# Optimization experiments

Hardware: AMD Instinct MI355X
Metric: run time of the kernel (lower is better)

## Reference

```python
import jax, jax.numpy as jnp
import numpy as np

N_NODES = 100000
N_EDGES = 600000
D_IN = 128   # num_features (== hidden due to source-code quirk)
D_H = 128    # hidden
BN_EPS = 1e-5
NORM_EPS = 1e-12


def _sage_conv(x, Wl, bl, Wr, src, dst):
    # mean aggregation of neighbor messages x_j (j = src) at target i (dst)
    msg_sum = jax.ops.segment_sum(x[src], dst, num_segments=N_NODES)          # [N, D]
    deg = jax.ops.segment_sum(jnp.ones_like(dst, dtype=x.dtype), dst,
                              num_segments=N_NODES)                            # [N]
    mean = msg_sum / jnp.maximum(deg, 1.0)[:, None]
    out = mean @ Wl.T + bl + x @ Wr.T   # lin_l(aggr) + lin_r(x)
    # F.normalize(out, p=2, dim=-1)
    norm = jnp.linalg.norm(out, axis=-1, keepdims=True)
    return out / jnp.maximum(norm, NORM_EPS)


def setup_inputs() -> dict:
    key = jax.random.key(0)
    ks = jax.random.split(key, 10)
    s1 = 1.0 / np.sqrt(D_IN)
    s2 = 1.0 / np.sqrt(D_H)
    x = jax.random.normal(ks[0], (N_NODES, D_IN), dtype=jnp.float32)
    edge_index = jax.random.randint(ks[1], (2, N_EDGES), 0, N_NODES, dtype=jnp.int64)
    return {
        "x": x,
        "edge_index": edge_index,
        "Wl1": jax.random.uniform(ks[2], (D_H, D_IN), jnp.float32, -s1, s1),
        "bl1": jax.random.uniform(ks[3], (D_H,), jnp.float32, -s1, s1),
        "Wr1": jax.random.uniform(ks[4], (D_H, D_IN), jnp.float32, -s1, s1),
        "Wl2": jax.random.uniform(ks[5], (D_H, D_H), jnp.float32, -s2, s2),
        "bl2": jax.random.uniform(ks[6], (D_H,), jnp.float32, -s2, s2),
        "Wr2": jax.random.uniform(ks[7], (D_H, D_H), jnp.float32, -s2, s2),
        "bn_gamma": jnp.ones((D_H,), jnp.float32),
        "bn_beta": jnp.zeros((D_H,), jnp.float32),
        "bn_mean": jax.random.normal(ks[8], (D_H,), jnp.float32) * 0.1,
        "bn_var": jnp.abs(jax.random.normal(ks[9], (D_H,), jnp.float32)) + 0.5,
    }


def reference(x, edge_index, Wl1, bl1, Wr1, Wl2, bl2, Wr2,
              bn_gamma, bn_beta, bn_mean, bn_var):
    src, dst = edge_index[0], edge_index[1]
    x1 = _sage_conv(x, Wl1, bl1, Wr1, src, dst)  # computed, unused (as in source)
    # transition applied to original x (source-code quirk): ReLU -> BN(eval) -> Dropout(id)
    h = jax.nn.relu(x)
    h = (h - bn_mean) * jax.lax.rsqrt(bn_var + BN_EPS) * bn_gamma + bn_beta
    x2 = _sage_conv(h, Wl2, bl2, Wr2, src, dst)
    return x2
```

## Files before the change

kernel.cpp:

```cpp
#include <hip/hip_runtime.h>
#include <math.h>

#define NN 100000
#define NE 600000
#define DD 128
#define NTILES 6250
#define TPB 8

typedef __attribute__((ext_vector_type(8))) __bf16 bf16x8;
typedef __attribute__((ext_vector_type(4))) float f32x4;

__device__ inline unsigned short f2bf(float f) {
    unsigned int u = __float_as_uint(f);
    unsigned int r = (u + 0x7fffu + ((u >> 16) & 1u)) >> 16;
    return (unsigned short)r;
}

__global__ void hist_kernel(const int* __restrict__ ei, int* __restrict__ counts) {
    int e = blockIdx.x * blockDim.x + threadIdx.x;
    if (e < NE) atomicAdd(&counts[ei[NE + e]], 1);
}

__global__ __launch_bounds__(256) void scan1_kernel(const int* __restrict__ counts,
                                                    int* __restrict__ offsets,
                                                    int* __restrict__ partials, int n) {
    __shared__ int tmp[256];
    int i = blockIdx.x * 256 + threadIdx.x;
    int v = (i < n) ? counts[i] : 0;
    tmp[threadIdx.x] = v;
    __syncthreads();
    for (int off = 1; off < 256; off <<= 1) {
        int t = (threadIdx.x >= off) ? tmp[threadIdx.x - off] : 0;
        __syncthreads();
        tmp[threadIdx.x] += t;
        __syncthreads();
    }
    if (i < n) offsets[i] = tmp[threadIdx.x] - v;
    if (threadIdx.x == 255) partials[blockIdx.x] = tmp[255];
}

__global__ __launch_bounds__(512) void scan2_kernel(int* __restrict__ partials, int nb) {
    __shared__ int tmp[512];
    int v = (threadIdx.x < nb) ? partials[threadIdx.x] : 0;
    tmp[threadIdx.x] = v;
    __syncthreads();
    for (int off = 1; off < 512; off <<= 1) {
        int t = (threadIdx.x >= off) ? tmp[threadIdx.x - off] : 0;
        __syncthreads();
        tmp[threadIdx.x] += t;
        __syncthreads();
    }
    if (threadIdx.x < nb) partials[threadIdx.x] = tmp[threadIdx.x] - v;
}

__global__ void scan3_kernel(int* __restrict__ offsets, int* __restrict__ cursor,
                             const int* __restrict__ partials, int n) {
    int i = blockIdx.x * 256 + threadIdx.x;
    if (i < n) {
        int o = offsets[i] + partials[blockIdx.x];
        offsets[i] = o;
        cursor[i]  = o;
    }
    if (i == 0) offsets[n] = NE;
}

__global__ void reorder_kernel(const int* __restrict__ ei, int* __restrict__ cursor,
                               int* __restrict__ ssrc) {
    int e = blockIdx.x * blockDim.x + threadIdx.x;
    if (e < NE) {
        int pos = atomicAdd(&cursor[ei[NE + e]], 1);
        ssrc[pos] = ei[e];
    }
}

__global__ void wt_stage_kernel(const float* __restrict__ Wl2,
                                const float* __restrict__ Wr2,
                                unsigned short* __restrict__ WT) {
    int t = blockIdx.x * blockDim.x + threadIdx.x;
    if (t >= DD * 256) return;
    int n = t >> 8;
    int k = t & 255;
    float v = (k < DD) ? Wl2[n * DD + k] : Wr2[n * DD + (k - DD)];
    WT[t] = f2bf(v);
}

__global__ __launch_bounds__(256) void aggregate_kernel(
    const float* __restrict__ x, const int* __restrict__ offsets,
    const int* __restrict__ ssrc,
    const float* __restrict__ bn_gamma, const float* __restrict__ bn_beta,
    const float* __restrict__ bn_mean, const float* __restrict__ bn_var,
    unsigned short* __restrict__ A)
{
    const int node = blockIdx.x * 8 + (threadIdx.x >> 5);
    const int l = threadIdx.x & 31;
    const int c = l * 4;

    const float4 bm = *(const float4*)(bn_mean  + c);
    const float4 bv = *(const float4*)(bn_var   + c);
    const float4 bg = *(const float4*)(bn_gamma + c);
    const float4 bb = *(const float4*)(bn_beta  + c);
    const float sc0 = rsqrtf(bv.x + 1e-5f) * bg.x;
    const float sc1 = rsqrtf(bv.y + 1e-5f) * bg.y;
    const float sc2 = rsqrtf(bv.z + 1e-5f) * bg.z;
    const float sc3 = rsqrtf(bv.w + 1e-5f) * bg.w;

    const int st = offsets[node], en = offsets[node + 1];
    const float* xb = x + c;

    float s0 = 0.f, s1 = 0.f, s2 = 0.f, s3 = 0.f;
    int j = st;
    for (; j + 4 <= en; j += 4) {
        const int4 ss = *(const int4*)(ssrc + j);
        float4 v0 = *(const float4*)(xb + (size_t)ss.x * DD);
        float4 v1 = *(const float4*)(xb + (size_t)ss.y * DD);
        float4 v2 = *(const float4*)(xb + (size_t)ss.z * DD);
        float4 v3 = *(const float4*)(xb + (size_t)ss.w * DD);
        s0 += fmaxf(v0.x, 0.f) + fmaxf(v1.x, 0.f) + fmaxf(v2.x, 0.f) + fmaxf(v3.x, 0.f);
        s1 += fmaxf(v0.y, 0.f) + fmaxf(v1.y, 0.f) + fmaxf(v2.y, 0.f) + fmaxf(v3.y, 0.f);
        s2 += fmaxf(v0.z, 0.f) + fmaxf(v1.z, 0.f) + fmaxf(v2.z, 0.f) + fmaxf(v3.z, 0.f);
        s3 += fmaxf(v0.w, 0.f) + fmaxf(v1.w, 0.f) + fmaxf(v2.w, 0.f) + fmaxf(v3.w, 0.f);
    }
    for (; j < en; ++j) {
        int s = ssrc[j];
        float4 v = *(const float4*)(xb + (size_t)s * DD);
        s0 += fmaxf(v.x, 0.f);
        s1 += fmaxf(v.y, 0.f);
        s2 += fmaxf(v.z, 0.f);
        s3 += fmaxf(v.w, 0.f);
    }

    const int deg = en - st;
    float m0, m1, m2, m3;
    if (deg > 0) {
        float inv = 1.0f / (float)deg;
        m0 = (s0 * inv - bm.x) * sc0 + bb.x;
        m1 = (s1 * inv - bm.y) * sc1 + bb.y;
        m2 = (s2 * inv - bm.z) * sc2 + bb.z;
        m3 = (s3 * inv - bm.w) * sc3 + bb.w;
    } else {
        m0 = m1 = m2 = m3 = 0.f;
    }

    const float4 xv = *(const float4*)(xb + (size_t)node * DD);
    float h0 = (fmaxf(xv.x, 0.f) - bm.x) * sc0 + bb.x;
    float h1 = (fmaxf(xv.y, 0.f) - bm.y) * sc1 + bb.y;
    float h2 = (fmaxf(xv.z, 0.f) - bm.z) * sc2 + bb.z;
    float h3 = (fmaxf(xv.w, 0.f) - bm.w) * sc3 + bb.w;

    unsigned short* arow = A + (size_t)node * 256;
    ushort4 mm; mm.x = f2bf(m0); mm.y = f2bf(m1); mm.z = f2bf(m2); mm.w = f2bf(m3);
    ushort4 hh; hh.x = f2bf(h0); hh.y = f2bf(h1); hh.z = f2bf(h2); hh.w = f2bf(h3);
    *(ushort4*)(arow + c)      = mm;
    *(ushort4*)(arow + DD + c) = hh;
}

__global__ __launch_bounds__(256) void mfma_gemm_norm_kernel(
    const unsigned short* __restrict__ A, const unsigned short* __restrict__ WT,
    const float* __restrict__ bl, float* __restrict__ out)
{
    __shared__ float partial[4][16];

    const int wave = threadIdx.x >> 6;
    const int l    = threadIdx.x & 63;
    const int r    = l & 15;
    const int seg  = l >> 4;
    const int c0   = wave * 32;

    bf16x8 bf0[8], bf1[8];
    {
        const unsigned short* bp0 = WT + (size_t)(c0 + r) * 256 + seg * 8;
        const unsigned short* bp1 = WT + (size_t)(c0 + 16 + r) * 256 + seg * 8;
#pragma unroll
        for (int kk = 0; kk < 8; ++kk) {
            bf0[kk] = *(const bf16x8*)(bp0 + kk * 32);
            bf1[kk] = *(const bf16x8*)(bp1 + kk * 32);
        }
    }
    const float bias0 = bl[c0 + r];
    const float bias1 = bl[c0 + 16 + r];

    const int tend = min((int)(blockIdx.x + 1) * TPB, NTILES);
#pragma unroll 1
    for (int t = blockIdx.x * TPB; t < tend; ++t) {
        const int row0 = t * 16;
        const unsigned short* ap = A + (size_t)(row0 + r) * 256 + seg * 8;

        bf16x8 af[8];
#pragma unroll
        for (int kk = 0; kk < 8; ++kk) af[kk] = *(const bf16x8*)(ap + kk * 32);

        f32x4 acc0 = {0.f, 0.f, 0.f, 0.f};
        f32x4 acc1 = {0.f, 0.f, 0.f, 0.f};
#pragma unroll
        for (int kk = 0; kk < 8; ++kk) {
            acc0 = __builtin_amdgcn_mfma_f32_16x16x32_bf16(af[kk], bf0[kk], acc0, 0, 0, 0);
            acc1 = __builtin_amdgcn_mfma_f32_16x16x32_bf16(af[kk], bf1[kk], acc1, 0, 0, 0);
        }

        float p[4];
#pragma unroll
        for (int q = 0; q < 4; ++q) {
            acc0[q] += bias0;
            acc1[q] += bias1;
            p[q] = acc0[q] * acc0[q] + acc1[q] * acc1[q];
        }
#pragma unroll
        for (int m = 1; m < 16; m <<= 1) {
#pragma unroll
            for (int q = 0; q < 4; ++q) p[q] += __shfl_xor(p[q], m);
        }
        if (r == 0) {
#pragma unroll
            for (int q = 0; q < 4; ++q) partial[wave][seg * 4 + q] = p[q];
        }
        __syncthreads();

#pragma unroll
        for (int q = 0; q < 4; ++q) {
            const int rr = seg * 4 + q;
            float s = partial[0][rr] + partial[1][rr] + partial[2][rr] + partial[3][rr];
            float inv = 1.0f / fmaxf(sqrtf(s), 1e-12f);
            float* orow = out + (size_t)(row0 + rr) * DD;
            orow[c0 + r]      = acc0[q] * inv;
            orow[c0 + 16 + r] = acc1[q] * inv;
        }
        __syncthreads();
    }
}

extern "C" void kernel_launch(void* const* d_in, const int* in_sizes, int n_in,
                              void* d_out, int out_size, void* d_ws, size_t ws_size,
                              hipStream_t stream) {
    const float* x        = (const float*)d_in[0];
    const int*   ei       = (const int*)d_in[1];
    const float* Wl2      = (const float*)d_in[5];
    const float* bl2      = (const float*)d_in[6];
    const float* Wr2      = (const float*)d_in[7];
    const float* bn_gamma = (const float*)d_in[8];
    const float* bn_beta  = (const float*)d_in[9];
    const float* bn_mean  = (const float*)d_in[10];
    const float* bn_var   = (const float*)d_in[11];
    float* out = (float*)d_out;

    unsigned short* A  = (unsigned short*)d_ws;
    unsigned short* WT = A + (size_t)NN * 256;
    int* counts   = (int*)(WT + DD * 256);
    int* offsets  = counts + NN;
    int* cursor   = offsets + NN + 1;
    int* partials = cursor + NN;
    int* ssrc     = partials + 512;

    const int nb_nodes = (NN + 255) / 256;
    const int nb_edges = (NE + 255) / 256;

    hipMemsetAsync(counts, 0, NN * sizeof(int), stream);
    hist_kernel<<<nb_edges, 256, 0, stream>>>(ei, counts);
    scan1_kernel<<<nb_nodes, 256, 0, stream>>>(counts, offsets, partials, NN);
    scan2_kernel<<<1, 512, 0, stream>>>(partials, nb_nodes);
    scan3_kernel<<<nb_nodes, 256, 0, stream>>>(offsets, cursor, partials, NN);
    reorder_kernel<<<nb_edges, 256, 0, stream>>>(ei, cursor, ssrc);
    wt_stage_kernel<<<(DD * 256 + 255) / 256, 256, 0, stream>>>(Wl2, Wr2, WT);
    aggregate_kernel<<<NN / 8, 256, 0, stream>>>(
        x, offsets, ssrc, bn_gamma, bn_beta, bn_mean, bn_var, A);
    const int gemm_blocks = (NTILES + TPB - 1) / TPB;
    mfma_gemm_norm_kernel<<<gemm_blocks, 256, 0, stream>>>(A, WT, bl2, out);
}
```

Baseline: 266.7 us.

## Fuse aggregation into MFMA GEMM via LDS and merge small preprocessing kernels

The neighbor-mean aggregation now writes its bf16 tile into swizzled shared memory, and the same block runs the MFMA GEMM and L2 normalisation on it. This removes the global A buffer round trip (100k x 256 bf16 written and read back). The histogram is merged with the weight staging, and the two tail scan kernels are merged, with each block summing its preceding partials itself. In exchange, every 16-row tile block reloads the full weight fragments from global/L2, and each block's scan prefix work grows linearly with block index.

```diff
diff --git a/kernel.cpp b/kernel.cpp
--- a/kernel.cpp
+++ b/kernel.cpp
@@ -5,7 +5,9 @@
 #define NE 600000
 #define DD 128
 #define NTILES 6250
-#define TPB 8
+#define NB_EDGES 2344
+#define NB_NODES 391
+#define NB_WT 128
 
 typedef __attribute__((ext_vector_type(8))) __bf16 bf16x8;
 typedef __attribute__((ext_vector_type(4))) float f32x4;
@@ -16,9 +18,22 @@
     return (unsigned short)r;
 }
 
-__global__ void hist_kernel(const int* __restrict__ ei, int* __restrict__ counts) {
-    int e = blockIdx.x * blockDim.x + threadIdx.x;
-    if (e < NE) atomicAdd(&counts[ei[NE + e]], 1);
+__global__ __launch_bounds__(256) void hist_wt_kernel(
+    const int* __restrict__ ei, int* __restrict__ counts,
+    const float* __restrict__ Wl2, const float* __restrict__ Wr2,
+    unsigned short* __restrict__ WT)
+{
+    const int b = blockIdx.x;
+    if (b < NB_EDGES) {
+        int e = b * 256 + threadIdx.x;
+        if (e < NE) atomicAdd(&counts[ei[NE + e]], 1);
+    } else {
+        int t = (b - NB_EDGES) * 256 + threadIdx.x;
+        int n = t >> 8;
+        int k = t & 255;
+        float v = (k < DD) ? Wl2[n * DD + k] : Wr2[n * DD + (k - DD)];
+        WT[t] = f2bf(v);
+    }
 }
 
 __global__ __launch_bounds__(256) void scan1_kernel(const int* __restrict__ counts,
@@ -39,29 +54,24 @@
     if (threadIdx.x == 255) partials[blockIdx.x] = tmp[255];
 }
 
-__global__ __launch_bounds__(512) void scan2_kernel(int* __restrict__ partials, int nb) {
-    __shared__ int tmp[512];
-    int v = (threadIdx.x < nb) ? partials[threadIdx.x] : 0;
-    tmp[threadIdx.x] = v;
-    __syncthreads();
-    for (int off = 1; off < 512; off <<= 1) {
-        int t = (threadIdx.x >= off) ? tmp[threadIdx.x - off] : 0;
-        __syncthreads();
-        tmp[threadIdx.x] += t;
-        __syncthreads();
-    }
-    if (threadIdx.x < nb) partials[threadIdx.x] = tmp[threadIdx.x] - v;
-}
-
-__global__ void scan3_kernel(int* __restrict__ offsets, int* __restrict__ cursor,
-                             const int* __restrict__ partials, int n) {
+__global__ __launch_bounds__(256) void scan23_kernel(int* __restrict__ offsets,
+                                                     int* __restrict__ cursor,
+                                                     const int* __restrict__ partials) {
+    __shared__ int sbase;
+    if (threadIdx.x == 0) sbase = 0;
+    __syncthreads();
+    int acc = 0;
+    for (int i = threadIdx.x; i < blockIdx.x; i += 256) acc += partials[i];
+    for (int off = 32; off > 0; off >>= 1) acc += __shfl_down(acc, off);
+    if ((threadIdx.x & 63) == 0 && acc != 0) atomicAdd(&sbase, acc);
+    __syncthreads();
     int i = blockIdx.x * 256 + threadIdx.x;
-    if (i < n) {
-        int o = offsets[i] + partials[blockIdx.x];
+    if (i < NN) {
+        int o = offsets[i] + sbase;
         offsets[i] = o;
         cursor[i]  = o;
     }
-    if (i == 0) offsets[n] = NE;
+    if (i == 0) offsets[NN] = NE;
 }
 
 __global__ void reorder_kernel(const int* __restrict__ ei, int* __restrict__ cursor,
@@ -73,95 +83,22 @@
     }
 }
 
-__global__ void wt_stage_kernel(const float* __restrict__ Wl2,
-                                const float* __restrict__ Wr2,
-                                unsigned short* __restrict__ WT) {
-    int t = blockIdx.x * blockDim.x + threadIdx.x;
-    if (t >= DD * 256) return;
-    int n = t >> 8;
-    int k = t & 255;
-    float v = (k < DD) ? Wl2[n * DD + k] : Wr2[n * DD + (k - DD)];
-    WT[t] = f2bf(v);
-}
-
-__global__ __launch_bounds__(256) void aggregate_kernel(
+__global__ __launch_bounds__(256) void fused_agg_gemm_kernel(
     const float* __restrict__ x, const int* __restrict__ offsets,
     const int* __restrict__ ssrc,
     const float* __restrict__ bn_gamma, const float* __restrict__ bn_beta,
     const float* __restrict__ bn_mean, const float* __restrict__ bn_var,
-    unsigned short* __restrict__ A)
+    const unsigned short* __restrict__ WT, const float* __restrict__ bl,
+    float* __restrict__ out)
 {
-    const int node = blockIdx.x * 8 + (threadIdx.x >> 5);
-    const int l = threadIdx.x & 31;
-    const int c = l * 4;
-
-    const float4 bm = *(const float4*)(bn_mean  + c);
-    const float4 bv = *(const float4*)(bn_var   + c);
-    const float4 bg = *(const float4*)(bn_gamma + c);
-    const float4 bb = *(const float4*)(bn_beta  + c);
-    const float sc0 = rsqrtf(bv.x + 1e-5f) * bg.x;
-    const float sc1 = rsqrtf(bv.y + 1e-5f) * bg.y;
-    const float sc2 = rsqrtf(bv.z + 1e-5f) * bg.z;
-    const float sc3 = rsqrtf(bv.w + 1e-5f) * bg.w;
-
-    const int st = offsets[node], en = offsets[node + 1];
-    const float* xb = x + c;
-
-    float s0 = 0.f, s1 = 0.f, s2 = 0.f, s3 = 0.f;
-    int j = st;
-    for (; j + 4 <= en; j += 4) {
-        const int4 ss = *(const int4*)(ssrc + j);
-        float4 v0 = *(const float4*)(xb + (size_t)ss.x * DD);
-        float4 v1 = *(const float4*)(xb + (size_t)ss.y * DD);
-        float4 v2 = *(const float4*)(xb + (size_t)ss.z * DD);
-        float4 v3 = *(const float4*)(xb + (size_t)ss.w * DD);
-        s0 += fmaxf(v0.x, 0.f) + fmaxf(v1.x, 0.f) + fmaxf(v2.x, 0.f) + fmaxf(v3.x, 0.f);
-        s1 += fmaxf(v0.y, 0.f) + fmaxf(v1.y, 0.f) + fmaxf(v2.y, 0.f) + fmaxf(v3.y, 0.f);
-        s2 += fmaxf(v0.z, 0.f) + fmaxf(v1.z, 0.f) + fmaxf(v2.z, 0.f) + fmaxf(v3.z, 0.f);
-        s3 += fmaxf(v0.w, 0.f) + fmaxf(v1.w, 0.f) + fmaxf(v2.w, 0.f) + fmaxf(v3.w, 0.f);
-    }
-    for (; j < en; ++j) {
-        int s = ssrc[j];
-        float4 v = *(const float4*)(xb + (size_t)s * DD);
-        s0 += fmaxf(v.x, 0.f);
-        s1 += fmaxf(v.y, 0.f);
-        s2 += fmaxf(v.z, 0.f);
-        s3 += fmaxf(v.w, 0.f);
-    }
-
-    const int deg = en - st;
-    float m0, m1, m2, m3;
-    if (deg > 0) {
-        float inv = 1.0f / (float)deg;
-        m0 = (s0 * inv - bm.x) * sc0 + bb.x;
-        m1 = (s1 * inv - bm.y) * sc1 + bb.y;
-        m2 = (s2 * inv - bm.z) * sc2 + bb.z;
-        m3 = (s3 * inv - bm.w) * sc3 + bb.w;
-    } else {
-        m0 = m1 = m2 = m3 = 0.f;
-    }
-
-    const float4 xv = *(const float4*)(xb + (size_t)node * DD);
-    float h0 = (fmaxf(xv.x, 0.f) - bm.x) * sc0 + bb.x;
-    float h1 = (fmaxf(xv.y, 0.f) - bm.y) * sc1 + bb.y;
-    float h2 = (fmaxf(xv.z, 0.f) - bm.z) * sc2 + bb.z;
-    float h3 = (fmaxf(xv.w, 0.f) - bm.w) * sc3 + bb.w;
-
-    unsigned short* arow = A + (size_t)node * 256;
-    ushort4 mm; mm.x = f2bf(m0); mm.y = f2bf(m1); mm.z = f2bf(m2); mm.w = f2bf(m3);
-    ushort4 hh; hh.x = f2bf(h0); hh.y = f2bf(h1); hh.z = f2bf(h2); hh.w = f2bf(h3);
-    *(ushort4*)(arow + c)      = mm;
-    *(ushort4*)(arow + DD + c) = hh;
-}
-
-__global__ __launch_bounds__(256) void mfma_gemm_norm_kernel(
-    const unsigned short* __restrict__ A, const unsigned short* __restrict__ WT,
-    const float* __restrict__ bl, float* __restrict__ out)
-{
+    __shared__ unsigned short ldsA[16 * 256];
     __shared__ float partial[4][16];
 
-    const int wave = threadIdx.x >> 6;
-    const int l    = threadIdx.x & 63;
+    const int tid  = threadIdx.x;
+    const int row0 = blockIdx.x * 16;
+
+    const int wave = tid >> 6;
+    const int l    = tid & 63;
     const int r    = l & 15;
     const int seg  = l >> 4;
     const int c0   = wave * 32;
@@ -179,52 +116,119 @@
     const float bias0 = bl[c0 + r];
     const float bias1 = bl[c0 + 16 + r];
 
-    const int tend = min((int)(blockIdx.x + 1) * TPB, NTILES);
+    {
+        const int g  = tid >> 5;
+        const int gl = tid & 31;
+        const int c  = gl * 4;
+
+        const float4 bm = *(const float4*)(bn_mean  + c);
+        const float4 bv = *(const float4*)(bn_var   + c);
+        const float4 bg = *(const float4*)(bn_gamma + c);
+        const float4 bb = *(const float4*)(bn_beta  + c);
+        const float sc0 = rsqrtf(bv.x + 1e-5f) * bg.x;
+        const float sc1 = rsqrtf(bv.y + 1e-5f) * bg.y;
+        const float sc2 = rsqrtf(bv.z + 1e-5f) * bg.z;
+        const float sc3 = rsqrtf(bv.w + 1e-5f) * bg.w;
+        const float* xb = x + c;
+
 #pragma unroll 1
-    for (int t = blockIdx.x * TPB; t < tend; ++t) {
-        const int row0 = t * 16;
-        const unsigned short* ap = A + (size_t)(row0 + r) * 256 + seg * 8;
-
-        bf16x8 af[8];
-#pragma unroll
-        for (int kk = 0; kk < 8; ++kk) af[kk] = *(const bf16x8*)(ap + kk * 32);
-
-        f32x4 acc0 = {0.f, 0.f, 0.f, 0.f};
-        f32x4 acc1 = {0.f, 0.f, 0.f, 0.f};
-#pragma unroll
-        for (int kk = 0; kk < 8; ++kk) {
-            acc0 = __builtin_amdgcn_mfma_f32_16x16x32_bf16(af[kk], bf0[kk], acc0, 0, 0, 0);
-            acc1 = __builtin_amdgcn_mfma_f32_16x16x32_bf16(af[kk], bf1[kk], acc1, 0, 0, 0);
+        for (int it = 0; it < 2; ++it) {
+            const int nt   = g * 2 + it;
+            const int node = row0 + nt;
+
+            const int st = offsets[node], en = offsets[node + 1];
+            float s0 = 0.f, s1 = 0.f, s2 = 0.f, s3 = 0.f;
+            int j = st;
+            for (; j + 4 <= en; j += 4) {
+                const int4 ss = *(const int4*)(ssrc + j);
+                float4 v0 = *(const float4*)(xb + (size_t)ss.x * DD);
+                float4 v1 = *(const float4*)(xb + (size_t)ss.y * DD);
+                float4 v2 = *(const float4*)(xb + (size_t)ss.z * DD);
+                float4 v3 = *(const float4*)(xb + (size_t)ss.w * DD);
+                s0 += fmaxf(v0.x, 0.f) + fmaxf(v1.x, 0.f) + fmaxf(v2.x, 0.f) + fmaxf(v3.x, 0.f);
+                s1 += fmaxf(v0.y, 0.f) + fmaxf(v1.y, 0.f) + fmaxf(v2.y, 0.f) + fmaxf(v3.y, 0.f);
+                s2 += fmaxf(v0.z, 0.f) + fmaxf(v1.z, 0.f) + fmaxf(v2.z, 0.f) + fmaxf(v3.z, 0.f);
+                s3 += fmaxf(v0.w, 0.f) + fmaxf(v1.w, 0.f) + fmaxf(v2.w, 0.f) + fmaxf(v3.w, 0.f);
+            }
+            for (; j < en; ++j) {
+                int s = ssrc[j];
+                float4 v = *(const float4*)(xb + (size_t)s * DD);
+                s0 += fmaxf(v.x, 0.f);
+                s1 += fmaxf(v.y, 0.f);
+                s2 += fmaxf(v.z, 0.f);
+                s3 += fmaxf(v.w, 0.f);
+            }
+
+            const int deg = en - st;
+            float m0, m1, m2, m3;
+            if (deg > 0) {
+                float inv = 1.0f / (float)deg;
+                m0 = (s0 * inv - bm.x) * sc0 + bb.x;
+                m1 = (s1 * inv - bm.y) * sc1 + bb.y;
+                m2 = (s2 * inv - bm.z) * sc2 + bb.z;
+                m3 = (s3 * inv - bm.w) * sc3 + bb.w;
+            } else {
+                m0 = m1 = m2 = m3 = 0.f;
+            }
+
+            const float4 xv = *(const float4*)(xb + (size_t)node * DD);
+            float h0 = (fmaxf(xv.x, 0.f) - bm.x) * sc0 + bb.x;
+            float h1 = (fmaxf(xv.y, 0.f) - bm.y) * sc1 + bb.y;
+            float h2 = (fmaxf(xv.z, 0.f) - bm.z) * sc2 + bb.z;
+            float h3 = (fmaxf(xv.w, 0.f) - bm.w) * sc3 + bb.w;
+
+            ushort4 mm; mm.x = f2bf(m0); mm.y = f2bf(m1); mm.z = f2bf(m2); mm.w = f2bf(m3);
+            ushort4 hh; hh.x = f2bf(h0); hh.y = f2bf(h1); hh.z = f2bf(h2); hh.w = f2bf(h3);
+
+            const int swz = (nt & 7) << 4;
+            char* rowp = (char*)ldsA + nt * 512;
+            *(ushort4*)(rowp + ((c * 2) ^ swz))       = mm;
+            *(ushort4*)(rowp + ((256 + c * 2) ^ swz)) = hh;
         }
-
-        float p[4];
-#pragma unroll
-        for (int q = 0; q < 4; ++q) {
-            acc0[q] += bias0;
-            acc1[q] += bias1;
-            p[q] = acc0[q] * acc0[q] + acc1[q] * acc1[q];
-        }
-#pragma unroll
-        for (int m = 1; m < 16; m <<= 1) {
-#pragma unroll
-            for (int q = 0; q < 4; ++q) p[q] += __shfl_xor(p[q], m);
-        }
-        if (r == 0) {
-#pragma unroll
-            for (int q = 0; q < 4; ++q) partial[wave][seg * 4 + q] = p[q];
-        }
-        __syncthreads();
-
-#pragma unroll
-        for (int q = 0; q < 4; ++q) {
-            const int rr = seg * 4 + q;
-            float s = partial[0][rr] + partial[1][rr] + partial[2][rr] + partial[3][rr];
-            float inv = 1.0f / fmaxf(sqrtf(s), 1e-12f);
-            float* orow = out + (size_t)(row0 + rr) * DD;
-            orow[c0 + r]      = acc0[q] * inv;
-            orow[c0 + 16 + r] = acc1[q] * inv;
-        }
-        __syncthreads();
+    }
+    __syncthreads();
+
+    bf16x8 af[8];
+#pragma unroll
+    for (int kk = 0; kk < 8; ++kk) {
+        const int o = (seg * 16 + kk * 64) ^ ((r & 7) << 4);
+        af[kk] = *(const bf16x8*)((const char*)ldsA + r * 512 + o);
+    }
+
+    f32x4 acc0 = {0.f, 0.f, 0.f, 0.f};
+    f32x4 acc1 = {0.f, 0.f, 0.f, 0.f};
+#pragma unroll
+    for (int kk = 0; kk < 8; ++kk) {
+        acc0 = __builtin_amdgcn_mfma_f32_16x16x32_bf16(af[kk], bf0[kk], acc0, 0, 0, 0);
+        acc1 = __builtin_amdgcn_mfma_f32_16x16x32_bf16(af[kk], bf1[kk], acc1, 0, 0, 0);
+    }
+
+    float p[4];
+#pragma unroll
+    for (int q = 0; q < 4; ++q) {
+        acc0[q] += bias0;
+        acc1[q] += bias1;
+        p[q] = acc0[q] * acc0[q] + acc1[q] * acc1[q];
+    }
+#pragma unroll
+    for (int m = 1; m < 16; m <<= 1) {
+#pragma unroll
+        for (int q = 0; q < 4; ++q) p[q] += __shfl_xor(p[q], m);
+    }
+    if (r == 0) {
+#pragma unroll
+        for (int q = 0; q < 4; ++q) partial[wave][seg * 4 + q] = p[q];
+    }
+    __syncthreads();
+
+#pragma unroll
+    for (int q = 0; q < 4; ++q) {
+        const int rr = seg * 4 + q;
+        float s = partial[0][rr] + partial[1][rr] + partial[2][rr] + partial[3][rr];
+        float inv = 1.0f / fmaxf(sqrtf(s), 1e-12f);
+        float* orow = out + (size_t)(row0 + rr) * DD;
+        orow[c0 + r]      = acc0[q] * inv;
+        orow[c0 + 16 + r] = acc1[q] * inv;
     }
 }
 
@@ -242,26 +246,18 @@
     const float* bn_var   = (const float*)d_in[11];
     float* out = (float*)d_out;
 
-    unsigned short* A  = (unsigned short*)d_ws;
-    unsigned short* WT = A + (size_t)NN * 256;
+    unsigned short* WT = (unsigned short*)d_ws;
     int* counts   = (int*)(WT + DD * 256);
     int* offsets  = counts + NN;
     int* cursor   = offsets + NN + 1;
     int* partials = cursor + NN;
     int* ssrc     = partials + 512;
 
-    const int nb_nodes = (NN + 255) / 256;
-    const int nb_edges = (NE + 255) / 256;
-
     hipMemsetAsync(counts, 0, NN * sizeof(int), stream);
-    hist_kernel<<<nb_edges, 256, 0, stream>>>(ei, counts);
-    scan1_kernel<<<nb_nodes, 256, 0, stream>>>(counts, offsets, partials, NN);
-    scan2_kernel<<<1, 512, 0, stream>>>(partials, nb_nodes);
-    scan3_kernel<<<nb_nodes, 256, 0, stream>>>(offsets, cursor, partials, NN);
-    reorder_kernel<<<nb_edges, 256, 0, stream>>>(ei, cursor, ssrc);
-    wt_stage_kernel<<<(DD * 256 + 255) / 256, 256, 0, stream>>>(Wl2, Wr2, WT);
-    aggregate_kernel<<<NN / 8, 256, 0, stream>>>(
-        x, offsets, ssrc, bn_gamma, bn_beta, bn_mean, bn_var, A);
-    const int gemm_blocks = (NTILES + TPB - 1) / TPB;
-    mfma_gemm_norm_kernel<<<gemm_blocks, 256, 0, stream>>>(A, WT, bl2, out);
-}
+    hist_wt_kernel<<<NB_EDGES + NB_WT, 256, 0, stream>>>(ei, counts, Wl2, Wr2, WT);
+    scan1_kernel<<<NB_NODES, 256, 0, stream>>>(counts, offsets, partials, NN);
+    scan23_kernel<<<NB_NODES, 256, 0, stream>>>(offsets, cursor, partials);
+    reorder_kernel<<<NB_EDGES, 256, 0, stream>>>(ei, cursor, ssrc);
+    fused_agg_gemm_kernel<<<NTILES, 256, 0, stream>>>(
+        x, offsets, ssrc, bn_gamma, bn_beta, bn_mean, bn_var, WT, bl2, out);
+}
```

New measurement: 285.4 us. +7.0%, slower.

## Fuse CSR build and weight staging into one cooperative kernel

Applied to the files above, without the earlier changes.

Replaces the memset, histogram, three scan kernels, the reorder kernel and the weight-staging kernel with a single cooperative launch of 512 blocks that uses grid-wide syncs between phases. The middle scan pass is dropped: each block now sums the partials of all earlier blocks directly. The aim is to cut launch overhead and inter-kernel gaps across seven small launches. In exchange it adds grid.sync costs, caps parallelism at 512 blocks, and the prefix sum per block grows with the block index.

```diff
diff --git a/kernel.cpp b/kernel.cpp
--- a/kernel.cpp
+++ b/kernel.cpp
@@ -1,11 +1,16 @@
 #include <hip/hip_runtime.h>
+#include <hip/hip_cooperative_groups.h>
 #include <math.h>
+
+namespace cg = cooperative_groups;
 
 #define NN 100000
 #define NE 600000
 #define DD 128
 #define NTILES 6250
 #define TPB 8
+#define NB_NODES 391
+#define COOP_BLOCKS 512
 
 typedef __attribute__((ext_vector_type(8))) __bf16 bf16x8;
 typedef __attribute__((ext_vector_type(4))) float f32x4;
@@ -16,72 +21,70 @@
     return (unsigned short)r;
 }
 
-__global__ void hist_kernel(const int* __restrict__ ei, int* __restrict__ counts) {
-    int e = blockIdx.x * blockDim.x + threadIdx.x;
-    if (e < NE) atomicAdd(&counts[ei[NE + e]], 1);
-}
-
-__global__ __launch_bounds__(256) void scan1_kernel(const int* __restrict__ counts,
-                                                    int* __restrict__ offsets,
-                                                    int* __restrict__ partials, int n) {
+__global__ __launch_bounds__(256) void edge_pipeline_kernel(
+    const int* __restrict__ ei,
+    const float* __restrict__ Wl2, const float* __restrict__ Wr2,
+    unsigned short* __restrict__ WT,
+    int* __restrict__ counts, int* __restrict__ offsets,
+    int* __restrict__ cursor, int* __restrict__ partials,
+    int* __restrict__ ssrc)
+{
+    cg::grid_group grid = cg::this_grid();
     __shared__ int tmp[256];
-    int i = blockIdx.x * 256 + threadIdx.x;
-    int v = (i < n) ? counts[i] : 0;
-    tmp[threadIdx.x] = v;
-    __syncthreads();
-    for (int off = 1; off < 256; off <<= 1) {
-        int t = (threadIdx.x >= off) ? tmp[threadIdx.x - off] : 0;
-        __syncthreads();
-        tmp[threadIdx.x] += t;
-        __syncthreads();
-    }
-    if (i < n) offsets[i] = tmp[threadIdx.x] - v;
-    if (threadIdx.x == 255) partials[blockIdx.x] = tmp[255];
-}
-
-__global__ __launch_bounds__(512) void scan2_kernel(int* __restrict__ partials, int nb) {
-    __shared__ int tmp[512];
-    int v = (threadIdx.x < nb) ? partials[threadIdx.x] : 0;
-    tmp[threadIdx.x] = v;
-    __syncthreads();
-    for (int off = 1; off < 512; off <<= 1) {
-        int t = (threadIdx.x >= off) ? tmp[threadIdx.x - off] : 0;
-        __syncthreads();
-        tmp[threadIdx.x] += t;
-        __syncthreads();
-    }
-    if (threadIdx.x < nb) partials[threadIdx.x] = tmp[threadIdx.x] - v;
-}
-
-__global__ void scan3_kernel(int* __restrict__ offsets, int* __restrict__ cursor,
-                             const int* __restrict__ partials, int n) {
-    int i = blockIdx.x * 256 + threadIdx.x;
-    if (i < n) {
-        int o = offsets[i] + partials[blockIdx.x];
-        offsets[i] = o;
-        cursor[i]  = o;
-    }
-    if (i == 0) offsets[n] = NE;
-}
-
-__global__ void reorder_kernel(const int* __restrict__ ei, int* __restrict__ cursor,
-                               int* __restrict__ ssrc) {
-    int e = blockIdx.x * blockDim.x + threadIdx.x;
-    if (e < NE) {
+    __shared__ int sbase;
+
+    const int tid  = blockIdx.x * 256 + threadIdx.x;
+    const int nthr = COOP_BLOCKS * 256;
+
+    for (int i = tid; i < NN; i += nthr) counts[i] = 0;
+    for (int t = tid; t < DD * 256; t += nthr) {
+        int n = t >> 8, k = t & 255;
+        float v = (k < DD) ? Wl2[n * DD + k] : Wr2[n * DD + (k - DD)];
+        WT[t] = f2bf(v);
+    }
+    grid.sync();
+
+    for (int e = tid; e < NE; e += nthr) atomicAdd(&counts[ei[NE + e]], 1);
+    grid.sync();
+
+    if (blockIdx.x < NB_NODES) {
+        int i = blockIdx.x * 256 + threadIdx.x;
+        int v = (i < NN) ? counts[i] : 0;
+        tmp[threadIdx.x] = v;
+        __syncthreads();
+        for (int off = 1; off < 256; off <<= 1) {
+            int t = (threadIdx.x >= off) ? tmp[threadIdx.x - off] : 0;
+            __syncthreads();
+            tmp[threadIdx.x] += t;
+            __syncthreads();
+        }
+        if (i < NN) offsets[i] = tmp[threadIdx.x] - v;
+        if (threadIdx.x == 255) partials[blockIdx.x] = tmp[255];
+    }
+    grid.sync();
+
+    if (blockIdx.x < NB_NODES) {
+        if (threadIdx.x == 0) sbase = 0;
+        __syncthreads();
+        int acc = 0;
+        for (int i = threadIdx.x; i < blockIdx.x; i += 256) acc += partials[i];
+        for (int off = 32; off > 0; off >>= 1) acc += __shfl_down(acc, off);
+        if ((threadIdx.x & 63) == 0 && acc != 0) atomicAdd(&sbase, acc);
+        __syncthreads();
+        int i = blockIdx.x * 256 + threadIdx.x;
+        if (i < NN) {
+            int o = offsets[i] + sbase;
+            offsets[i] = o;
+            cursor[i]  = o;
+        }
+        if (i == 0) offsets[NN] = NE;
+    }
+    grid.sync();
+
+    for (int e = tid; e < NE; e += nthr) {
         int pos = atomicAdd(&cursor[ei[NE + e]], 1);
         ssrc[pos] = ei[e];
     }
-}
-
-__global__ void wt_stage_kernel(const float* __restrict__ Wl2,
-                                const float* __restrict__ Wr2,
-                                unsigned short* __restrict__ WT) {
-    int t = blockIdx.x * blockDim.x + threadIdx.x;
-    if (t >= DD * 256) return;
-    int n = t >> 8;
-    int k = t & 255;
-    float v = (k < DD) ? Wl2[n * DD + k] : Wr2[n * DD + (k - DD)];
-    WT[t] = f2bf(v);
 }
 
 __global__ __launch_bounds__(256) void aggregate_kernel(
@@ -250,16 +253,15 @@
     int* partials = cursor + NN;
     int* ssrc     = partials + 512;
 
-    const int nb_nodes = (NN + 255) / 256;
-    const int nb_edges = (NE + 255) / 256;
-
-    hipMemsetAsync(counts, 0, NN * sizeof(int), stream);
-    hist_kernel<<<nb_edges, 256, 0, stream>>>(ei, counts);
-    scan1_kernel<<<nb_nodes, 256, 0, stream>>>(counts, offsets, partials, NN);
-    scan2_kernel<<<1, 512, 0, stream>>>(partials, nb_nodes);
-    scan3_kernel<<<nb_nodes, 256, 0, stream>>>(offsets, cursor, partials, NN);
-    reorder_kernel<<<nb_edges, 256, 0, stream>>>(ei, cursor, ssrc);
-    wt_stage_kernel<<<(DD * 256 + 255) / 256, 256, 0, stream>>>(Wl2, Wr2, WT);
+    {
+        void* args[] = {
+            (void*)&ei, (void*)&Wl2, (void*)&Wr2, (void*)&WT,
+            (void*)&counts, (void*)&offsets, (void*)&cursor,
+            (void*)&partials, (void*)&ssrc
+        };
+        hipLaunchCooperativeKernel((const void*)edge_pipeline_kernel,
+                                   dim3(COOP_BLOCKS), dim3(256), args, 0, stream);
+    }
     aggregate_kernel<<<NN / 8, 256, 0, stream>>>(
         x, offsets, ssrc, bn_gamma, bn_beta, bn_mean, bn_var, A);
     const int gemm_blocks = (NTILES + TPB - 1) / TPB;
```

Result: slower. 488.9 us (+83.3%).
